# Performance work log

Hardware: AMD Instinct MI355X
Metric: run time of the kernel (lower is better)

The kernel has to match this reference:

```python
import jax, jax.numpy as jnp
import numpy as np

EPS_GN = 1e-5
EPS_ATTN = 1e-6
HEADS = 4
DIM_HEAD = 32
GROUPS = 32  # min(32, channels=128)


def group_norm(x, weight, bias, groups=GROUPS, eps=EPS_GN):
    # x: [b, c, h, w]
    b, c, h, w = x.shape
    xg = x.reshape(b, groups, c // groups, h, w)
    mean = xg.mean(axis=(2, 3, 4), keepdims=True)
    var = xg.var(axis=(2, 3, 4), keepdims=True)
    xg = (xg - mean) * jax.lax.rsqrt(var + eps)
    x = xg.reshape(b, c, h, w)
    return x * weight[None, :, None, None] + bias[None, :, None, None]


def conv1x1(x, w):
    # x: [b, c, h, w], w: [out, in] -> [b, out, h, w]
    return jnp.einsum('bchw,oc->bohw', x, w)


def setup_inputs() -> dict:
    key = jax.random.key(0)
    ks = jax.random.split(key, 6)
    b, c, h, w = 16, 128, 128, 128
    inner = HEADS * DIM_HEAD  # 128
    x = jax.random.normal(ks[0], (b, c, h, w), dtype=jnp.float32)
    gn1_w = jnp.ones((c,), jnp.float32) + 0.02 * jax.random.normal(ks[1], (c,), jnp.float32)
    gn1_b = 0.02 * jax.random.normal(ks[2], (c,), jnp.float32)
    w_qkv = jax.random.normal(ks[3], (inner * 3, c), jnp.float32) / np.sqrt(c)
    w_out = jax.random.normal(ks[4], (c, inner), jnp.float32) / np.sqrt(inner)
    gn2_w = jnp.ones((c,), jnp.float32) + 0.02 * jax.random.normal(ks[5], (c,), jnp.float32)
    gn2_b = jnp.zeros((c,), jnp.float32)
    return {"x": x, "gn1_w": gn1_w, "gn1_b": gn1_b, "w_qkv": w_qkv,
            "w_out": w_out, "gn2_w": gn2_w, "gn2_b": gn2_b}


def reference(x, gn1_w, gn1_b, w_qkv, w_out, gn2_w, gn2_b):
    b, c, h, w = x.shape
    residual = x
    xn = group_norm(x, gn1_w, gn1_b)
    qkv = conv1x1(xn, w_qkv)                      # [b, 3*inner, h, w]
    q, k, v = jnp.split(qkv, 3, axis=1)
    # 'b (heads d) h w -> b heads (h w) d'
    def to_tokens(t):
        return t.reshape(b, HEADS, DIM_HEAD, h * w).transpose(0, 1, 3, 2)
    q, k, v = to_tokens(q), to_tokens(k), to_tokens(v)
    q = jax.nn.elu(q) + 1.0
    k = jax.nn.elu(k) + 1.0
    k_sum = k.sum(axis=2)                          # [b, heads, d]
    kv = jnp.einsum('bhnd,bhne->bhde', k, v)       # [b, heads, d, d]
    qk_sum = jnp.einsum('bhnd,bhd->bhn', q, k_sum) # [b, heads, n]
    qkv_out = jnp.einsum('bhnd,bhde->bhne', q, kv) # [b, heads, n, d]
    out = qkv_out / (qk_sum[..., None] + EPS_ATTN)
    # 'b heads (h w) d -> b (heads d) h w'
    out = out.transpose(0, 1, 3, 2).reshape(b, HEADS * DIM_HEAD, h, w)
    out = conv1x1(out, w_out)
    out = group_norm(out, gn2_w, gn2_b)
    return out + residual
```

## Files before the change

### kernel.cpp

```cpp
#include <hip/hip_runtime.h>

#define B_   16
#define C_   128
#define HW_  16384

typedef __attribute__((ext_vector_type(4))) float  floatx4;
typedef __attribute__((ext_vector_type(8))) short  short8;
typedef __attribute__((ext_vector_type(4))) short  short4v;

static __device__ __forceinline__ unsigned short f2bf(float f){
  unsigned int u = __float_as_uint(f);
  u += 0x7FFFu + ((u >> 16) & 1u);
  return (unsigned short)(u >> 16);
}
static __device__ __forceinline__ float bf2f(unsigned short h){
  return __uint_as_float(((unsigned int)h) << 16);
}
static __device__ __forceinline__ float elu1(float v){
  return v > 0.f ? v + 1.f : __expf(v);
}
static __device__ __forceinline__ int keyx(int n){ return ((n >> 1) & 7) ^ ((n >> 4) & 7); }

__global__ __launch_bounds__(512) void k_xprep(const float* __restrict__ x,
    unsigned short* __restrict__ xT, float* __restrict__ gn1part){
  int blk = blockIdx.x;
  int b = blk >> 6, tile = blk & 63;
  int n0 = tile * 256;
  __shared__ unsigned short XS[32768];
  int t = threadIdx.x, w = t >> 6, l = t & 63;
  float sk[4], sk2[4];
  #pragma unroll
  for (int k = 0; k < 4; ++k){ sk[k] = 0.f; sk2[k] = 0.f; }
  #pragma unroll
  for (int k = 0; k < 4; ++k){
    float4 f4[4];
    #pragma unroll
    for (int j = 0; j < 4; ++j){
      int c = 16*w + 4*k + j;
      f4[j] = *(const float4*)(x + ((size_t)(b*128 + c))*HW_ + n0 + 4*l);
    }
    #pragma unroll
    for (int j = 0; j < 4; ++j){
      sk[k]  += f4[j].x + f4[j].y + f4[j].z + f4[j].w;
      sk2[k] += f4[j].x*f4[j].x + f4[j].y*f4[j].y + f4[j].z*f4[j].z + f4[j].w*f4[j].w;
    }
    int c0 = 16*w + 4*k, cs = c0 >> 3, co = c0 & 7;
    #pragma unroll
    for (int i = 0; i < 4; ++i){
      int n = 4*l + i;
      short4v p;
      #pragma unroll
      for (int j = 0; j < 4; ++j) p[j] = (short)f2bf(((const float*)&f4[j])[i]);
      *(short4v*)(XS + n*128 + (((cs ^ keyx(n)) << 3) + co)) = p;
    }
  }
  #pragma unroll
  for (int k = 0; k < 4; ++k){
    float a = sk[k], q = sk2[k];
    #pragma unroll
    for (int o = 32; o; o >>= 1){ a += __shfl_down(a, o); q += __shfl_down(q, o); }
    if (l == 0){
      gn1part[((size_t)blk)*64 + (4*w + k)*2 + 0] = a;
      gn1part[((size_t)blk)*64 + (4*w + k)*2 + 1] = q;
    }
  }
  __syncthreads();
  unsigned short* dst = xT + ((size_t)blk)*32768;
  for (int it = 0; it < 8; ++it){
    int slot = t + it*512;
    *(short8*)(dst + slot*8) = *(const short8*)(XS + slot*8);
  }
}

__global__ __launch_bounds__(64) void k_gn1fin(const float* __restrict__ gn1part,
    float* __restrict__ mean, float* __restrict__ rstd){
  int bg = blockIdx.x;
  int b = bg >> 5, g = bg & 31, l = threadIdx.x;
  const float* p = gn1part + ((size_t)(b*64 + l))*64 + g*2;
  float s = p[0], s2 = p[1];
  #pragma unroll
  for (int o = 32; o; o >>= 1){ s += __shfl_down(s, o); s2 += __shfl_down(s2, o); }
  if (l == 0){
    float m = s * (1.f/65536.f);
    float var = s2 * (1.f/65536.f) - m*m;
    mean[bg] = m; rstd[bg] = rsqrtf(var + 1e-5f);
  }
}

__global__ __launch_bounds__(64) void k_fold(const float* __restrict__ wqkv, const float* __restrict__ wout,
    const float* __restrict__ g1w, const float* __restrict__ g1b,
    const float* __restrict__ mean, const float* __restrict__ rstd,
    unsigned short* __restrict__ wqp, float* __restrict__ bias, unsigned short* __restrict__ woutb){
  int i = blockIdx.x, l = threadIdx.x;
  if (i < 6144){
    int b = i / 384, o = i % 384;
    float bsum = 0.f;
    #pragma unroll
    for (int j = 0; j < 2; ++j){
      int c = l*2 + j, g = c >> 2;
      float m = mean[b*32 + g], r = rstd[b*32 + g];
      float A  = r * g1w[c];
      float Bc = g1b[c] - m * A;
      float wv = wqkv[o*128 + c];
      wqp[((size_t)(b*384 + o))*128 + c] = f2bf(wv * A);
      bsum += wv * Bc;
    }
    #pragma unroll
    for (int o2 = 32; o2; o2 >>= 1) bsum += __shfl_down(bsum, o2);
    if (l == 0) bias[b*384 + o] = bsum;
  } else {
    int r = i - 6144;
    #pragma unroll
    for (int j = 0; j < 2; ++j){ int c = l*2 + j; woutb[r*128 + c] = f2bf(wout[r*128 + c]); }
  }
}

__global__ __launch_bounds__(512) void k_kv(const unsigned short* __restrict__ xT,
    const unsigned short* __restrict__ wqp, const float* __restrict__ bias,
    float* __restrict__ kvpart, float* __restrict__ ksumpart){
  int blk = blockIdx.x;
  int b = blk >> 7, nt = blk & 127;
  __shared__ unsigned short S[32768];
  int t = threadIdx.x, w = t >> 6, lane = t & 63, lr = lane & 15, lk = lane >> 4;
  const unsigned short* src = xT + ((size_t)(b*64 + (nt >> 1)))*32768 + (nt & 1)*16384;
  for (int it = 0; it < 4; ++it){
    int slot = t + it*512;
    *(short8*)(S + slot*8) = *(const short8*)(src + slot*8);
  }
  __syncthreads();
  short8 afr[2][4]; float biasr[2][4];
  #pragma unroll
  for (int rt = 0; rt < 2; ++rt){
    int o = 128 + rt*128 + w*16;
    #pragma unroll
    for (int ks = 0; ks < 4; ++ks)
      afr[rt][ks] = *(const short8*)(wqp + ((size_t)(b*384 + o + lr))*128 + ks*32 + lk*8);
    #pragma unroll
    for (int r = 0; r < 4; ++r) biasr[rt][r] = bias[b*384 + o + lk*4 + r];
  }
  short4v kpk[8], vpk[8];
  for (int ct = 0; ct < 8; ++ct){
    int nr = ct*16 + lr;
    int kn = keyx(nr);
    short8 bfr[4];
    #pragma unroll
    for (int ks = 0; ks < 4; ++ks)
      bfr[ks] = *(const short8*)(S + nr*128 + (((ks*4 + lk) ^ kn) << 3));
    #pragma unroll
    for (int rt = 0; rt < 2; ++rt){
      floatx4 acc = {0.f,0.f,0.f,0.f};
      #pragma unroll
      for (int ks = 0; ks < 4; ++ks)
        acc = __builtin_amdgcn_mfma_f32_16x16x32_bf16(afr[rt][ks], bfr[ks], acc, 0,0,0);
      short4v pk;
      #pragma unroll
      for (int r = 0; r < 4; ++r){
        float v = acc[r] + biasr[rt][r];
        if (rt == 0) v = elu1(v);
        pk[r] = (short)f2bf(v);
      }
      if (rt == 0) kpk[ct] = pk; else vpk[ct] = pk;
    }
  }
  __syncthreads();
  for (int ct = 0; ct < 8; ++ct){
    int n = ct*16 + lr;
    #pragma unroll
    for (int r = 0; r < 4; ++r){
      int c = w*16 + lk*4 + r;
      int key = (c >> 1) & 7;
      int off = c*128 + ((((n >> 3) ^ key) << 3) + (n & 7));
      S[off]         = (unsigned short)kpk[ct][r];
      S[16384 + off] = (unsigned short)vpk[ct][r];
    }
  }
  __syncthreads();
  short8 ones;
  #pragma unroll
  for (int j = 0; j < 8; ++j) ones[j] = (short)0x3F80;
  #pragma unroll
  for (int j = 0; j < 2; ++j){
    int m = w + 8*j;
    int h = m >> 2, dt = (m >> 1) & 1, et = m & 1;
    int arow = h*32 + dt*16 + lr, brow = h*32 + et*16 + lr;
    int akey = (lr >> 1) & 7;
    floatx4 acc = {0.f,0.f,0.f,0.f}, ks_acc = {0.f,0.f,0.f,0.f};
    #pragma unroll
    for (int ks = 0; ks < 4; ++ks){
      short8 ka = *(const short8*)(S + arow*128 + (((ks*4 + lk) ^ akey) << 3));
      short8 vb = *(const short8*)(S + 16384 + brow*128 + (((ks*4 + lk) ^ akey) << 3));
      acc = __builtin_amdgcn_mfma_f32_16x16x32_bf16(ka, vb, acc, 0,0,0);
      if (et == 0) ks_acc = __builtin_amdgcn_mfma_f32_16x16x32_bf16(ka, ones, ks_acc, 0,0,0);
    }
    float* kvp = kvpart + ((size_t)((b*128 + nt)*4 + h))*1024;
    #pragma unroll
    for (int r = 0; r < 4; ++r)
      kvp[(dt*16 + lk*4 + r)*32 + et*16 + lr] = acc[r];
    if (et == 0 && lr == 0){
      float* ksp = ksumpart + ((size_t)((b*128 + nt)*4 + h))*32;
      #pragma unroll
      for (int r = 0; r < 4; ++r) ksp[dt*16 + lk*4 + r] = ks_acc[r];
    }
  }
}

__global__ __launch_bounds__(256) void k_kvmfold(const float* __restrict__ kvpart, const float* __restrict__ ksumpart,
    const unsigned short* __restrict__ woutb, unsigned short* __restrict__ Mb, float* __restrict__ ksumF){
  int bh = blockIdx.x, t = threadIdx.x;
  int b = bh >> 2, h = bh & 3;
  __shared__ float kvL[1024];
  for (int i = t; i < 1024; i += 256){
    float s = 0.f;
    for (int nt = 0; nt < 128; ++nt) s += kvpart[((size_t)((b*128 + nt)*4 + h))*1024 + i];
    kvL[i] = s;
  }
  if (t < 32){
    float s = 0.f;
    for (int nt = 0; nt < 128; ++nt) s += ksumpart[((size_t)((b*128 + nt)*4 + h))*32 + t];
    ksumF[b*128 + h*32 + t] = s;
  }
  __syncthreads();
  int o = t >> 1, d0 = (t & 1)*16;
  float w2row[32];
  #pragma unroll
  for (int e = 0; e < 32; ++e) w2row[e] = bf2f(woutb[o*128 + h*32 + e]);
  for (int dd = 0; dd < 16; ++dd){
    int d = d0 + dd;
    float s = 0.f;
    #pragma unroll
    for (int e = 0; e < 32; ++e) s += w2row[e] * kvL[d*32 + e];
    Mb[((size_t)b)*16384 + o*128 + h*32 + d] = f2bf(s);
  }
}

__global__ __launch_bounds__(256) void k_attn2(const unsigned short* __restrict__ xT,
    const unsigned short* __restrict__ wqp, const float* __restrict__ bias,
    const float* __restrict__ ksumF, const unsigned short* __restrict__ Mb,
    unsigned short* __restrict__ hbT, float* __restrict__ gn2part){
  int blk = blockIdx.x;
  int b = blk >> 7, t128 = blk & 127;
  __shared__ unsigned short S[16384];
  int t = threadIdx.x, w = t >> 6, lane = t & 63, lr = lane & 15, lk = lane >> 4;
  int rg = w >> 1, cg = w & 1;
  const unsigned short* src = xT + ((size_t)(b*64 + (t128 >> 1)))*32768 + (t128 & 1)*16384;
  for (int it = 0; it < 8; ++it){
    int slot = t + it*256;
    *(short8*)(S + slot*8) = *(const short8*)(src + slot*8);
  }
  short8 afr[4][4]; float biasq[4][4], ksL[4][4];
  #pragma unroll
  for (int rtl = 0; rtl < 4; ++rtl){
    int o = rg*64 + rtl*16;
    #pragma unroll
    for (int ks = 0; ks < 4; ++ks)
      afr[rtl][ks] = *(const short8*)(wqp + ((size_t)(b*384 + o + lr))*128 + ks*32 + lk*8);
    #pragma unroll
    for (int r = 0; r < 4; ++r){
      biasq[rtl][r] = bias[b*384 + o + lk*4 + r];
      ksL[rtl][r]   = ksumF[b*128 + o + lk*4 + r];
    }
  }
  __syncthreads();
  short4v qpk[4][4];
  #pragma unroll
  for (int ctl = 0; ctl < 4; ++ctl){
    int nr = cg*64 + ctl*16 + lr;
    int kn = keyx(nr);
    short8 bfr[4];
    #pragma unroll
    for (int ks = 0; ks < 4; ++ks)
      bfr[ks] = *(const short8*)(S + nr*128 + (((ks*4 + lk) ^ kn) << 3));
    float qv[4][4];
    #pragma unroll
    for (int rtl = 0; rtl < 4; ++rtl){
      floatx4 acc = {0.f,0.f,0.f,0.f};
      #pragma unroll
      for (int ks = 0; ks < 4; ++ks)
        acc = __builtin_amdgcn_mfma_f32_16x16x32_bf16(afr[rtl][ks], bfr[ks], acc, 0,0,0);
      #pragma unroll
      for (int r = 0; r < 4; ++r) qv[rtl][r] = elu1(acc[r] + biasq[rtl][r]);
    }
    #pragma unroll
    for (int hh = 0; hh < 2; ++hh){
      float p = 0.f;
      #pragma unroll
      for (int rr = 0; rr < 2; ++rr)
        #pragma unroll
        for (int r = 0; r < 4; ++r) p += ksL[2*hh + rr][r] * qv[2*hh + rr][r];
      p += __shfl_xor(p, 16);
      p += __shfl_xor(p, 32);
      float inv = 1.f / (p + 1e-6f);
      #pragma unroll
      for (int rr = 0; rr < 2; ++rr)
        #pragma unroll
        for (int r = 0; r < 4; ++r) qpk[2*hh + rr][ctl][r] = (short)f2bf(qv[2*hh + rr][r] * inv);
    }
  }
  __syncthreads();
  #pragma unroll
  for (int rtl = 0; rtl < 4; ++rtl){
    int c0 = rg*64 + rtl*16 + lk*4;
    #pragma unroll
    for (int ctl = 0; ctl < 4; ++ctl){
      int n = cg*64 + ctl*16 + lr;
      *(short4v*)(S + n*128 + ((((c0 >> 3) ^ (n & 7)) << 3) + (c0 & 7))) = qpk[rtl][ctl];
    }
  }
  __syncthreads();
  short8 afr2[4][4];
  #pragma unroll
  for (int rtl = 0; rtl < 4; ++rtl)
    #pragma unroll
    for (int ks = 0; ks < 4; ++ks)
      afr2[rtl][ks] = *(const short8*)(Mb + ((size_t)b)*16384 + (size_t)(rg*64 + rtl*16 + lr)*128 + ks*32 + lk*8);
  float gs[4][4], gq[4][4];
  #pragma unroll
  for (int rtl = 0; rtl < 4; ++rtl)
    #pragma unroll
    for (int r = 0; r < 4; ++r){ gs[rtl][r] = 0.f; gq[rtl][r] = 0.f; }
  #pragma unroll
  for (int ctl = 0; ctl < 4; ++ctl){
    int nr = cg*64 + ctl*16 + lr;
    short8 bfr[4];
    #pragma unroll
    for (int ks = 0; ks < 4; ++ks)
      bfr[ks] = *(const short8*)(S + nr*128 + (((ks*4 + lk) ^ (nr & 7)) << 3));
    #pragma unroll
    for (int rtl = 0; rtl < 4; ++rtl){
      floatx4 acc = {0.f,0.f,0.f,0.f};
      #pragma unroll
      for (int ks = 0; ks < 4; ++ks)
        acc = __builtin_amdgcn_mfma_f32_16x16x32_bf16(afr2[rtl][ks], bfr[ks], acc, 0,0,0);
      #pragma unroll
      for (int r = 0; r < 4; ++r){
        float hv = acc[r];
        int c = rg*64 + rtl*16 + lk*4 + r;
        hbT[(size_t)blk*16384 + c*128 + nr] = f2bf(hv);
        gs[rtl][r] += hv; gq[rtl][r] += hv * hv;
      }
    }
  }
  #pragma unroll
  for (int m = 1; m < 16; m <<= 1)
    #pragma unroll
    for (int rtl = 0; rtl < 4; ++rtl)
      #pragma unroll
      for (int r = 0; r < 4; ++r){ gs[rtl][r] += __shfl_xor(gs[rtl][r], m); gq[rtl][r] += __shfl_xor(gq[rtl][r], m); }
  if (lr == 0){
    #pragma unroll
    for (int rtl = 0; rtl < 4; ++rtl)
      #pragma unroll
      for (int r = 0; r < 4; ++r){
        int c = rg*64 + rtl*16 + lk*4 + r;
        gn2part[((size_t)(blk*2 + cg)*128 + c)*2 + 0] = gs[rtl][r];
        gn2part[((size_t)(blk*2 + cg)*128 + c)*2 + 1] = gq[rtl][r];
      }
  }
}

__global__ __launch_bounds__(64) void k_gn2stats(const float* __restrict__ gn2part,
    float* __restrict__ mean, float* __restrict__ rstd){
  int b = blockIdx.x >> 5, g = blockIdx.x & 31;
  int lane = threadIdx.x;
  float s = 0.f, s2 = 0.f;
  #pragma unroll
  for (int tt = 0; tt < 2; ++tt){
    int t128 = lane + tt*64;
    #pragma unroll
    for (int cgi = 0; cgi < 2; ++cgi)
      #pragma unroll
      for (int j = 0; j < 4; ++j){
        const float* p = gn2part + ((size_t)((b*128 + t128)*2 + cgi)*128 + g*4 + j)*2;
        s += p[0]; s2 += p[1];
      }
  }
  #pragma unroll
  for (int o = 32; o; o >>= 1){ s += __shfl_down(s, o); s2 += __shfl_down(s2, o); }
  if (lane == 0){
    float m = s * (1.f/65536.f);
    float var = s2 * (1.f/65536.f) - m*m;
    mean[blockIdx.x] = m; rstd[blockIdx.x] = rsqrtf(var + 1e-5f);
  }
}

__global__ __launch_bounds__(256) void k_final(const unsigned short* __restrict__ hbT,
    const unsigned short* __restrict__ xT, float* __restrict__ out,
    const float* __restrict__ mean, const float* __restrict__ rstd,
    const float* __restrict__ g2w, const float* __restrict__ g2b){
  int blk = blockIdx.x;
  int b = blk >> 7, t128 = blk & 127;
  __shared__ unsigned short XS[16384];
  int t = threadIdx.x;
  const unsigned short* src = xT + ((size_t)(b*64 + (t128 >> 1)))*32768 + (t128 & 1)*16384;
  for (int it = 0; it < 8; ++it){
    int slot = t + it*256;
    *(short8*)(XS + slot*8) = *(const short8*)(src + slot*8);
  }
  __syncthreads();
  const unsigned short* hsrc = hbT + (size_t)blk*16384;
  for (int it = 0; it < 8; ++it){
    int idx = t + it*256;
    int c = idx >> 4, oct = idx & 15;
    int bg = b*32 + (c >> 2);
    float m = mean[bg], r = rstd[bg];
    float sc = r * g2w[c], sh = g2b[c] - m * sc;
    short8 hv = *(const short8*)(hsrc + c*128 + oct*8);
    float ov[8];
    #pragma unroll
    for (int j = 0; j < 8; ++j){
      int n = oct*8 + j;
      unsigned short xv = XS[n*128 + ((((c >> 3) ^ keyx(n)) << 3) + (c & 7))];
      ov[j] = bf2f((unsigned short)hv[j])*sc + sh + bf2f(xv);
    }
    float* op = out + ((size_t)(b*128 + c))*HW_ + t128*128 + oct*8;
    float4 o0, o1;
    o0.x = ov[0]; o0.y = ov[1]; o0.z = ov[2]; o0.w = ov[3];
    o1.x = ov[4]; o1.y = ov[5]; o1.z = ov[6]; o1.w = ov[7];
    *(float4*)op = o0; *(float4*)(op + 4) = o1;
  }
}

extern "C" void kernel_launch(void* const* d_in, const int* in_sizes, int n_in,
                              void* d_out, int out_size, void* d_ws, size_t ws_size,
                              hipStream_t stream){
  const float* x    = (const float*)d_in[0];
  const float* g1w  = (const float*)d_in[1];
  const float* g1b  = (const float*)d_in[2];
  const float* wqkv = (const float*)d_in[3];
  const float* wout = (const float*)d_in[4];
  const float* g2w  = (const float*)d_in[5];
  const float* g2b  = (const float*)d_in[6];
  char* ws = (char*)d_ws;
  (void)in_sizes; (void)n_in; (void)out_size; (void)ws_size;

  float* gn1part  = (float*)(ws + 0);
  float* gn1_mean = (float*)(ws + 262144);
  float* gn1_rstd = (float*)(ws + 264192);
  float* gn2_mean = (float*)(ws + 266240);
  float* gn2_rstd = (float*)(ws + 268288);
  float* bias     = (float*)(ws + 270336);
  unsigned short* woutb = (unsigned short*)(ws + 294912);
  float* ksumF    = (float*)(ws + 327680);
  unsigned short* Mb = (unsigned short*)(ws + 335872);
  unsigned short* wqp = (unsigned short*)(ws + 860160);
  float* ksumpart = (float*)(ws + 2433024);
  float* kvpart   = (float*)(ws + 4194304);
  float* gn2part  = (float*)(ws + 37748736);
  unsigned short* xT  = (unsigned short*)(ws + 41943040);
  unsigned short* hbT = (unsigned short*)(ws + 109051904);

  k_xprep<<<dim3(1024), dim3(512), 0, stream>>>(x, xT, gn1part);
  k_gn1fin<<<dim3(512), dim3(64), 0, stream>>>(gn1part, gn1_mean, gn1_rstd);
  k_fold<<<dim3(6272), dim3(64), 0, stream>>>(wqkv, wout, g1w, g1b, gn1_mean, gn1_rstd, wqp, bias, woutb);
  k_kv<<<dim3(2048), dim3(512), 0, stream>>>(xT, wqp, bias, kvpart, ksumpart);
  k_kvmfold<<<dim3(64), dim3(256), 0, stream>>>(kvpart, ksumpart, woutb, Mb, ksumF);
  k_attn2<<<dim3(2048), dim3(256), 0, stream>>>(xT, wqp, bias, ksumF, Mb, hbT, gn2part);
  k_gn2stats<<<dim3(512), dim3(64), 0, stream>>>(gn2part, gn2_mean, gn2_rstd);
  k_final<<<dim3(2048), dim3(256), 0, stream>>>(hbT, xT, (float*)d_out, gn2_mean, gn2_rstd, g2w, g2b);
}
```

Before: 241.1 us.

## Restructure attn2 so each wave owns 32 tokens and drops shared-memory staging

k_attn2 now gives each wave its own 32 token columns across all 128 channels. It reads its B fragments straight from global xT and moves the normalized q between MFMA layouts with lane shuffles, so the shared-memory round trip and the block barriers go away. The hbT output is written in an MFMA-fragment layout with vectorized short4 stores instead of scattered 2-byte stores, and k_final stages hbT through shared memory to undo that layout. Per-wave GN2 partials grow to four rows per block, which changes the k_gn2stats indexing and the workspace offsets. In exchange, every wave reloads the full wqp and Mb weight matrices, and k_final uses twice the shared memory.

```diff
diff --git a/kernel.cpp b/kernel.cpp
--- a/kernel.cpp
+++ b/kernel.cpp
@@ -7,6 +7,8 @@
 typedef __attribute__((ext_vector_type(4))) float  floatx4;
 typedef __attribute__((ext_vector_type(8))) short  short8;
 typedef __attribute__((ext_vector_type(4))) short  short4v;
+
+typedef union { unsigned int u[4]; short8 s; } pk8_t;
 
 static __device__ __forceinline__ unsigned short f2bf(float f){
   unsigned int u = __float_as_uint(f);
@@ -15,6 +17,9 @@
 }
 static __device__ __forceinline__ float bf2f(unsigned short h){
   return __uint_as_float(((unsigned int)h) << 16);
+}
+static __device__ __forceinline__ unsigned int pack2bf(float lo, float hi){
+  return (unsigned int)f2bf(lo) | ((unsigned int)f2bf(hi) << 16);
 }
 static __device__ __forceinline__ float elu1(float v){
   return v > 0.f ? v + 1.f : __expf(v);
@@ -239,144 +244,133 @@
     unsigned short* __restrict__ hbT, float* __restrict__ gn2part){
   int blk = blockIdx.x;
   int b = blk >> 7, t128 = blk & 127;
-  __shared__ unsigned short S[16384];
   int t = threadIdx.x, w = t >> 6, lane = t & 63, lr = lane & 15, lk = lane >> 4;
-  int rg = w >> 1, cg = w & 1;
   const unsigned short* src = xT + ((size_t)(b*64 + (t128 >> 1)))*32768 + (t128 & 1)*16384;
-  for (int it = 0; it < 8; ++it){
-    int slot = t + it*256;
-    *(short8*)(S + slot*8) = *(const short8*)(src + slot*8);
-  }
-  short8 afr[4][4]; float biasq[4][4], ksL[4][4];
-  #pragma unroll
-  for (int rtl = 0; rtl < 4; ++rtl){
-    int o = rg*64 + rtl*16;
+
+  short8 xq[2][4];
+  #pragma unroll
+  for (int nt = 0; nt < 2; ++nt){
+    int nr = w*32 + nt*16 + lr;
+    int kn = keyx(nr);
     #pragma unroll
     for (int ks = 0; ks < 4; ++ks)
-      afr[rtl][ks] = *(const short8*)(wqp + ((size_t)(b*384 + o + lr))*128 + ks*32 + lk*8);
-    #pragma unroll
-    for (int r = 0; r < 4; ++r){
-      biasq[rtl][r] = bias[b*384 + o + lk*4 + r];
-      ksL[rtl][r]   = ksumF[b*128 + o + lk*4 + r];
-    }
-  }
-  __syncthreads();
-  short4v qpk[4][4];
-  #pragma unroll
-  for (int ctl = 0; ctl < 4; ++ctl){
-    int nr = cg*64 + ctl*16 + lr;
-    int kn = keyx(nr);
-    short8 bfr[4];
-    #pragma unroll
-    for (int ks = 0; ks < 4; ++ks)
-      bfr[ks] = *(const short8*)(S + nr*128 + (((ks*4 + lk) ^ kn) << 3));
-    float qv[4][4];
-    #pragma unroll
-    for (int rtl = 0; rtl < 4; ++rtl){
-      floatx4 acc = {0.f,0.f,0.f,0.f};
+      xq[nt][ks] = *(const short8*)(src + nr*128 + (((ks*4 + lk) ^ kn) << 3));
+  }
+
+  unsigned int qp[2][8][2];
+  #pragma unroll
+  for (int h = 0; h < 4; ++h){
+    short8 afr[2][4]; float bq_[2][4], ks_[2][4];
+    #pragma unroll
+    for (int rr = 0; rr < 2; ++rr){
+      int rtl = h*2 + rr;
       #pragma unroll
       for (int ks = 0; ks < 4; ++ks)
-        acc = __builtin_amdgcn_mfma_f32_16x16x32_bf16(afr[rtl][ks], bfr[ks], acc, 0,0,0);
-      #pragma unroll
-      for (int r = 0; r < 4; ++r) qv[rtl][r] = elu1(acc[r] + biasq[rtl][r]);
-    }
-    #pragma unroll
-    for (int hh = 0; hh < 2; ++hh){
-      float p = 0.f;
-      #pragma unroll
-      for (int rr = 0; rr < 2; ++rr)
+        afr[rr][ks] = *(const short8*)(wqp + ((size_t)(b*384 + rtl*16 + lr))*128 + ks*32 + lk*8);
+      #pragma unroll
+      for (int r = 0; r < 4; ++r){
+        int c = rtl*16 + lk*4 + r;
+        bq_[rr][r] = bias[b*384 + c];
+        ks_[rr][r] = ksumF[b*128 + c];
+      }
+    }
+    #pragma unroll
+    for (int nt = 0; nt < 2; ++nt){
+      float qv[2][4]; float p = 0.f;
+      #pragma unroll
+      for (int rr = 0; rr < 2; ++rr){
+        floatx4 acc = {0.f,0.f,0.f,0.f};
         #pragma unroll
-        for (int r = 0; r < 4; ++r) p += ksL[2*hh + rr][r] * qv[2*hh + rr][r];
+        for (int ks = 0; ks < 4; ++ks)
+          acc = __builtin_amdgcn_mfma_f32_16x16x32_bf16(afr[rr][ks], xq[nt][ks], acc, 0,0,0);
+        #pragma unroll
+        for (int r = 0; r < 4; ++r){
+          qv[rr][r] = elu1(acc[r] + bq_[rr][r]);
+          p += ks_[rr][r] * qv[rr][r];
+        }
+      }
       p += __shfl_xor(p, 16);
       p += __shfl_xor(p, 32);
       float inv = 1.f / (p + 1e-6f);
       #pragma unroll
-      for (int rr = 0; rr < 2; ++rr)
-        #pragma unroll
-        for (int r = 0; r < 4; ++r) qpk[2*hh + rr][ctl][r] = (short)f2bf(qv[2*hh + rr][r] * inv);
-    }
-  }
-  __syncthreads();
-  #pragma unroll
-  for (int rtl = 0; rtl < 4; ++rtl){
-    int c0 = rg*64 + rtl*16 + lk*4;
-    #pragma unroll
-    for (int ctl = 0; ctl < 4; ++ctl){
-      int n = cg*64 + ctl*16 + lr;
-      *(short4v*)(S + n*128 + ((((c0 >> 3) ^ (n & 7)) << 3) + (c0 & 7))) = qpk[rtl][ctl];
-    }
-  }
-  __syncthreads();
-  short8 afr2[4][4];
-  #pragma unroll
-  for (int rtl = 0; rtl < 4; ++rtl)
+      for (int rr = 0; rr < 2; ++rr){
+        int rtl = h*2 + rr;
+        qp[nt][rtl][0] = pack2bf(qv[rr][0]*inv, qv[rr][1]*inv);
+        qp[nt][rtl][1] = pack2bf(qv[rr][2]*inv, qv[rr][3]*inv);
+      }
+    }
+  }
+
+  short8 bq[2][4];
+  #pragma unroll
+  for (int nt = 0; nt < 2; ++nt)
+    #pragma unroll
+    for (int ks = 0; ks < 4; ++ks){
+      pk8_t pk;
+      #pragma unroll
+      for (int m = 0; m < 4; ++m){
+        int slane = (((lk*2 + (m >> 1)) & 3) << 4) | lr;
+        unsigned int c0 = (unsigned int)__shfl((int)qp[nt][2*ks    ][m & 1], slane);
+        unsigned int c1 = (unsigned int)__shfl((int)qp[nt][2*ks + 1][m & 1], slane);
+        pk.u[m] = (lk & 2) ? c1 : c0;
+      }
+      bq[nt][ks] = pk.s;
+    }
+
+  const unsigned short* mb = Mb + (size_t)b * 16384;
+  float* gpp = gn2part + ((size_t)(blk*4 + w)) * 256;
+  unsigned short* hdst = hbT + (size_t)blk * 16384;
+  #pragma unroll
+  for (int rtl = 0; rtl < 8; ++rtl){
+    short8 afr2[4];
     #pragma unroll
     for (int ks = 0; ks < 4; ++ks)
-      afr2[rtl][ks] = *(const short8*)(Mb + ((size_t)b)*16384 + (size_t)(rg*64 + rtl*16 + lr)*128 + ks*32 + lk*8);
-  float gs[4][4], gq[4][4];
-  #pragma unroll
-  for (int rtl = 0; rtl < 4; ++rtl)
-    #pragma unroll
-    for (int r = 0; r < 4; ++r){ gs[rtl][r] = 0.f; gq[rtl][r] = 0.f; }
-  #pragma unroll
-  for (int ctl = 0; ctl < 4; ++ctl){
-    int nr = cg*64 + ctl*16 + lr;
-    short8 bfr[4];
-    #pragma unroll
-    for (int ks = 0; ks < 4; ++ks)
-      bfr[ks] = *(const short8*)(S + nr*128 + (((ks*4 + lk) ^ (nr & 7)) << 3));
-    #pragma unroll
-    for (int rtl = 0; rtl < 4; ++rtl){
+      afr2[ks] = *(const short8*)(mb + (rtl*16 + lr)*128 + ks*32 + lk*8);
+    float gs[4] = {0,0,0,0}, gq[4] = {0,0,0,0};
+    #pragma unroll
+    for (int nt = 0; nt < 2; ++nt){
       floatx4 acc = {0.f,0.f,0.f,0.f};
       #pragma unroll
       for (int ks = 0; ks < 4; ++ks)
-        acc = __builtin_amdgcn_mfma_f32_16x16x32_bf16(afr2[rtl][ks], bfr[ks], acc, 0,0,0);
+        acc = __builtin_amdgcn_mfma_f32_16x16x32_bf16(afr2[ks], bq[nt][ks], acc, 0,0,0);
+      short4v pk;
       #pragma unroll
       for (int r = 0; r < 4; ++r){
         float hv = acc[r];
-        int c = rg*64 + rtl*16 + lk*4 + r;
-        hbT[(size_t)blk*16384 + c*128 + nr] = f2bf(hv);
-        gs[rtl][r] += hv; gq[rtl][r] += hv * hv;
-      }
-    }
-  }
-  #pragma unroll
-  for (int m = 1; m < 16; m <<= 1)
-    #pragma unroll
-    for (int rtl = 0; rtl < 4; ++rtl)
-      #pragma unroll
-      for (int r = 0; r < 4; ++r){ gs[rtl][r] += __shfl_xor(gs[rtl][r], m); gq[rtl][r] += __shfl_xor(gq[rtl][r], m); }
-  if (lr == 0){
-    #pragma unroll
-    for (int rtl = 0; rtl < 4; ++rtl)
+        pk[r] = (short)f2bf(hv);
+        gs[r] += hv; gq[r] += hv*hv;
+      }
+      *(short4v*)(hdst + (((w*8 + rtl)*2 + nt) << 8) + lane*4) = pk;
+    }
+    #pragma unroll
+    for (int m = 1; m < 16; m <<= 1)
+      #pragma unroll
+      for (int r = 0; r < 4; ++r){ gs[r] += __shfl_xor(gs[r], m); gq[r] += __shfl_xor(gq[r], m); }
+    if (lr == 0){
       #pragma unroll
       for (int r = 0; r < 4; ++r){
-        int c = rg*64 + rtl*16 + lk*4 + r;
-        gn2part[((size_t)(blk*2 + cg)*128 + c)*2 + 0] = gs[rtl][r];
-        gn2part[((size_t)(blk*2 + cg)*128 + c)*2 + 1] = gq[rtl][r];
-      }
+        int c = rtl*16 + lk*4 + r;
+        gpp[c*2 + 0] = gs[r];
+        gpp[c*2 + 1] = gq[r];
+      }
+    }
   }
 }
 
 __global__ __launch_bounds__(64) void k_gn2stats(const float* __restrict__ gn2part,
     float* __restrict__ mean, float* __restrict__ rstd){
   int b = blockIdx.x >> 5, g = blockIdx.x & 31;
-  int lane = threadIdx.x;
+  int l = threadIdx.x;
   float s = 0.f, s2 = 0.f;
-  #pragma unroll
-  for (int tt = 0; tt < 2; ++tt){
-    int t128 = lane + tt*64;
-    #pragma unroll
-    for (int cgi = 0; cgi < 2; ++cgi)
-      #pragma unroll
-      for (int j = 0; j < 4; ++j){
-        const float* p = gn2part + ((size_t)((b*128 + t128)*2 + cgi)*128 + g*4 + j)*2;
-        s += p[0]; s2 += p[1];
-      }
+  for (int rr = 0; rr < 8; ++rr){
+    int row = l + rr*64;
+    const float* p = gn2part + ((size_t)(b*512 + row))*256 + g*8;
+    #pragma unroll
+    for (int j = 0; j < 4; ++j){ s += p[j*2]; s2 += p[j*2 + 1]; }
   }
   #pragma unroll
   for (int o = 32; o; o >>= 1){ s += __shfl_down(s, o); s2 += __shfl_down(s2, o); }
-  if (lane == 0){
+  if (l == 0){
     float m = s * (1.f/65536.f);
     float var = s2 * (1.f/65536.f) - m*m;
     mean[blockIdx.x] = m; rstd[blockIdx.x] = rsqrtf(var + 1e-5f);
@@ -389,28 +383,32 @@
     const float* __restrict__ g2w, const float* __restrict__ g2b){
   int blk = blockIdx.x;
   int b = blk >> 7, t128 = blk & 127;
+  __shared__ unsigned short HS[16384];
   __shared__ unsigned short XS[16384];
   int t = threadIdx.x;
-  const unsigned short* src = xT + ((size_t)(b*64 + (t128 >> 1)))*32768 + (t128 & 1)*16384;
+  const unsigned short* hsrc = hbT + (size_t)blk*16384;
+  const unsigned short* xsrc = xT + ((size_t)(b*64 + (t128 >> 1)))*32768 + (t128 & 1)*16384;
   for (int it = 0; it < 8; ++it){
     int slot = t + it*256;
-    *(short8*)(XS + slot*8) = *(const short8*)(src + slot*8);
-  }
-  __syncthreads();
-  const unsigned short* hsrc = hbT + (size_t)blk*16384;
+    *(short8*)(HS + slot*8) = *(const short8*)(hsrc + slot*8);
+    *(short8*)(XS + slot*8) = *(const short8*)(xsrc + slot*8);
+  }
+  __syncthreads();
   for (int it = 0; it < 8; ++it){
     int idx = t + it*256;
     int c = idx >> 4, oct = idx & 15;
     int bg = b*32 + (c >> 2);
     float m = mean[bg], r = rstd[bg];
     float sc = r * g2w[c], sh = g2b[c] - m * sc;
-    short8 hv = *(const short8*)(hsrc + c*128 + oct*8);
+    int hbase = ((oct >> 2)*8 + (c >> 4))*512 + ((oct >> 1) & 1)*256
+              + ((c >> 2) & 3)*64 + ((oct & 1)*8)*4 + (c & 3);
     float ov[8];
     #pragma unroll
     for (int j = 0; j < 8; ++j){
       int n = oct*8 + j;
+      float hv = bf2f(HS[hbase + j*4]);
       unsigned short xv = XS[n*128 + ((((c >> 3) ^ keyx(n)) << 3) + (c & 7))];
-      ov[j] = bf2f((unsigned short)hv[j])*sc + sh + bf2f(xv);
+      ov[j] = hv*sc + sh + bf2f(xv);
     }
     float* op = out + ((size_t)(b*128 + c))*HW_ + t128*128 + oct*8;
     float4 o0, o1;
@@ -446,8 +444,8 @@
   float* ksumpart = (float*)(ws + 2433024);
   float* kvpart   = (float*)(ws + 4194304);
   float* gn2part  = (float*)(ws + 37748736);
-  unsigned short* xT  = (unsigned short*)(ws + 41943040);
-  unsigned short* hbT = (unsigned short*)(ws + 109051904);
+  unsigned short* xT  = (unsigned short*)(ws + 46137344);
+  unsigned short* hbT = (unsigned short*)(ws + 113246208);
 
   k_xprep<<<dim3(1024), dim3(512), 0, stream>>>(x, xT, gn1part);
   k_gn1fin<<<dim3(512), dim3(64), 0, stream>>>(gn1part, gn1_mean, gn1_rstd);
```

Measured after the change: 256.7 us. 6.5% more time.

## Process two token tiles per attn2 block and write hbT in fragment layout

Applied to the files above, without the earlier changes.

k_attn2 now handles two 128-token tiles per block (1024 blocks), reusing the weight fragments loaded into registers and prefetching the second tile's xT into registers while the first is computed. The hbT output is written as contiguous short4 per-lane fragments instead of scattered 2-byte stores, and k_final stages hbT through LDS and unpacks that layout. The workspace offsets for xT and hbT are shifted. The cost is more LDS per attn2 block (64KB) and more registers, which lowers occupancy, plus an extra LDS buffer in k_final.

```diff
diff --git a/kernel.cpp b/kernel.cpp
--- a/kernel.cpp
+++ b/kernel.cpp
@@ -238,15 +238,21 @@
     const float* __restrict__ ksumF, const unsigned short* __restrict__ Mb,
     unsigned short* __restrict__ hbT, float* __restrict__ gn2part){
   int blk = blockIdx.x;
-  int b = blk >> 7, t128 = blk & 127;
-  __shared__ unsigned short S[16384];
+  int b = blk >> 6, pair = blk & 63;
+  __shared__ unsigned short S[2][16384];
   int t = threadIdx.x, w = t >> 6, lane = t & 63, lr = lane & 15, lk = lane >> 4;
   int rg = w >> 1, cg = w & 1;
-  const unsigned short* src = xT + ((size_t)(b*64 + (t128 >> 1)))*32768 + (t128 & 1)*16384;
-  for (int it = 0; it < 8; ++it){
-    int slot = t + it*256;
-    *(short8*)(S + slot*8) = *(const short8*)(src + slot*8);
-  }
+
+  const unsigned short* src = xT + ((size_t)(b*64 + pair))*32768;
+  #pragma unroll
+  for (int i = 0; i < 8; ++i){
+    short8 v = *(const short8*)(src + (t + i*256)*8);
+    *(short8*)(&S[0][(t + i*256)*8]) = v;
+  }
+  short8 st[8];
+  #pragma unroll
+  for (int i = 0; i < 8; ++i) st[i] = *(const short8*)(src + 16384 + (t + i*256)*8);
+
   short8 afr[4][4]; float biasq[4][4], ksL[4][4];
   #pragma unroll
   for (int rtl = 0; rtl < 4; ++rtl){
@@ -260,101 +266,112 @@
       ksL[rtl][r]   = ksumF[b*128 + o + lk*4 + r];
     }
   }
-  __syncthreads();
-  short4v qpk[4][4];
-  #pragma unroll
-  for (int ctl = 0; ctl < 4; ++ctl){
-    int nr = cg*64 + ctl*16 + lr;
-    int kn = keyx(nr);
-    short8 bfr[4];
-    #pragma unroll
-    for (int ks = 0; ks < 4; ++ks)
-      bfr[ks] = *(const short8*)(S + nr*128 + (((ks*4 + lk) ^ kn) << 3));
-    float qv[4][4];
-    #pragma unroll
-    for (int rtl = 0; rtl < 4; ++rtl){
-      floatx4 acc = {0.f,0.f,0.f,0.f};
-      #pragma unroll
-      for (int ks = 0; ks < 4; ++ks)
-        acc = __builtin_amdgcn_mfma_f32_16x16x32_bf16(afr[rtl][ks], bfr[ks], acc, 0,0,0);
-      #pragma unroll
-      for (int r = 0; r < 4; ++r) qv[rtl][r] = elu1(acc[r] + biasq[rtl][r]);
-    }
-    #pragma unroll
-    for (int hh = 0; hh < 2; ++hh){
-      float p = 0.f;
-      #pragma unroll
-      for (int rr = 0; rr < 2; ++rr)
-        #pragma unroll
-        for (int r = 0; r < 4; ++r) p += ksL[2*hh + rr][r] * qv[2*hh + rr][r];
-      p += __shfl_xor(p, 16);
-      p += __shfl_xor(p, 32);
-      float inv = 1.f / (p + 1e-6f);
-      #pragma unroll
-      for (int rr = 0; rr < 2; ++rr)
-        #pragma unroll
-        for (int r = 0; r < 4; ++r) qpk[2*hh + rr][ctl][r] = (short)f2bf(qv[2*hh + rr][r] * inv);
-    }
-  }
-  __syncthreads();
-  #pragma unroll
-  for (int rtl = 0; rtl < 4; ++rtl){
-    int c0 = rg*64 + rtl*16 + lk*4;
-    #pragma unroll
-    for (int ctl = 0; ctl < 4; ++ctl){
-      int n = cg*64 + ctl*16 + lr;
-      *(short4v*)(S + n*128 + ((((c0 >> 3) ^ (n & 7)) << 3) + (c0 & 7))) = qpk[rtl][ctl];
-    }
-  }
-  __syncthreads();
   short8 afr2[4][4];
   #pragma unroll
   for (int rtl = 0; rtl < 4; ++rtl)
     #pragma unroll
     for (int ks = 0; ks < 4; ++ks)
       afr2[rtl][ks] = *(const short8*)(Mb + ((size_t)b)*16384 + (size_t)(rg*64 + rtl*16 + lr)*128 + ks*32 + lk*8);
-  float gs[4][4], gq[4][4];
-  #pragma unroll
-  for (int rtl = 0; rtl < 4; ++rtl)
-    #pragma unroll
-    for (int r = 0; r < 4; ++r){ gs[rtl][r] = 0.f; gq[rtl][r] = 0.f; }
-  #pragma unroll
-  for (int ctl = 0; ctl < 4; ++ctl){
-    int nr = cg*64 + ctl*16 + lr;
-    short8 bfr[4];
-    #pragma unroll
-    for (int ks = 0; ks < 4; ++ks)
-      bfr[ks] = *(const short8*)(S + nr*128 + (((ks*4 + lk) ^ (nr & 7)) << 3));
+  __syncthreads();
+
+  for (int tt = 0; tt < 2; ++tt){
+    unsigned short* Sc = &S[tt][0];
+    short4v qpk[4][4];
+    #pragma unroll
+    for (int ctl = 0; ctl < 4; ++ctl){
+      int nr = cg*64 + ctl*16 + lr;
+      int kn = keyx(nr);
+      short8 bfr[4];
+      #pragma unroll
+      for (int ks = 0; ks < 4; ++ks)
+        bfr[ks] = *(const short8*)(Sc + nr*128 + (((ks*4 + lk) ^ kn) << 3));
+      float qv[4][4];
+      #pragma unroll
+      for (int rtl = 0; rtl < 4; ++rtl){
+        floatx4 acc = {0.f,0.f,0.f,0.f};
+        #pragma unroll
+        for (int ks = 0; ks < 4; ++ks)
+          acc = __builtin_amdgcn_mfma_f32_16x16x32_bf16(afr[rtl][ks], bfr[ks], acc, 0,0,0);
+        #pragma unroll
+        for (int r = 0; r < 4; ++r) qv[rtl][r] = elu1(acc[r] + biasq[rtl][r]);
+      }
+      #pragma unroll
+      for (int hh = 0; hh < 2; ++hh){
+        float p = 0.f;
+        #pragma unroll
+        for (int rr = 0; rr < 2; ++rr)
+          #pragma unroll
+          for (int r = 0; r < 4; ++r) p += ksL[2*hh + rr][r] * qv[2*hh + rr][r];
+        p += __shfl_xor(p, 16);
+        p += __shfl_xor(p, 32);
+        float inv = 1.f / (p + 1e-6f);
+        #pragma unroll
+        for (int rr = 0; rr < 2; ++rr)
+          #pragma unroll
+          for (int r = 0; r < 4; ++r) qpk[2*hh + rr][ctl][r] = (short)f2bf(qv[2*hh + rr][r] * inv);
+      }
+    }
+    if (tt == 0){
+      #pragma unroll
+      for (int i = 0; i < 8; ++i) *(short8*)(&S[1][(t + i*256)*8]) = st[i];
+    }
+    __syncthreads();
     #pragma unroll
     for (int rtl = 0; rtl < 4; ++rtl){
-      floatx4 acc = {0.f,0.f,0.f,0.f};
+      int c0 = rg*64 + rtl*16 + lk*4;
+      #pragma unroll
+      for (int ctl = 0; ctl < 4; ++ctl){
+        int n = cg*64 + ctl*16 + lr;
+        *(short4v*)(Sc + n*128 + ((((c0 >> 3) ^ (n & 7)) << 3) + (c0 & 7))) = qpk[rtl][ctl];
+      }
+    }
+    __syncthreads();
+    int t128g = pair*2 + tt;
+    unsigned short* hdst = hbT + ((size_t)(b*128 + t128g))*16384;
+    float gs[4][4], gq[4][4];
+    #pragma unroll
+    for (int rtl = 0; rtl < 4; ++rtl)
+      #pragma unroll
+      for (int r = 0; r < 4; ++r){ gs[rtl][r] = 0.f; gq[rtl][r] = 0.f; }
+    #pragma unroll
+    for (int ctl = 0; ctl < 4; ++ctl){
+      int nr = cg*64 + ctl*16 + lr;
+      short8 bfr[4];
       #pragma unroll
       for (int ks = 0; ks < 4; ++ks)
-        acc = __builtin_amdgcn_mfma_f32_16x16x32_bf16(afr2[rtl][ks], bfr[ks], acc, 0,0,0);
-      #pragma unroll
-      for (int r = 0; r < 4; ++r){
-        float hv = acc[r];
-        int c = rg*64 + rtl*16 + lk*4 + r;
-        hbT[(size_t)blk*16384 + c*128 + nr] = f2bf(hv);
-        gs[rtl][r] += hv; gq[rtl][r] += hv * hv;
-      }
-    }
-  }
-  #pragma unroll
-  for (int m = 1; m < 16; m <<= 1)
-    #pragma unroll
-    for (int rtl = 0; rtl < 4; ++rtl)
-      #pragma unroll
-      for (int r = 0; r < 4; ++r){ gs[rtl][r] += __shfl_xor(gs[rtl][r], m); gq[rtl][r] += __shfl_xor(gq[rtl][r], m); }
-  if (lr == 0){
-    #pragma unroll
-    for (int rtl = 0; rtl < 4; ++rtl)
-      #pragma unroll
-      for (int r = 0; r < 4; ++r){
-        int c = rg*64 + rtl*16 + lk*4 + r;
-        gn2part[((size_t)(blk*2 + cg)*128 + c)*2 + 0] = gs[rtl][r];
-        gn2part[((size_t)(blk*2 + cg)*128 + c)*2 + 1] = gq[rtl][r];
-      }
+        bfr[ks] = *(const short8*)(Sc + nr*128 + (((ks*4 + lk) ^ (nr & 7)) << 3));
+      #pragma unroll
+      for (int rtl = 0; rtl < 4; ++rtl){
+        floatx4 acc = {0.f,0.f,0.f,0.f};
+        #pragma unroll
+        for (int ks = 0; ks < 4; ++ks)
+          acc = __builtin_amdgcn_mfma_f32_16x16x32_bf16(afr2[rtl][ks], bfr[ks], acc, 0,0,0);
+        short4v pk;
+        #pragma unroll
+        for (int r = 0; r < 4; ++r){
+          float hv = acc[r];
+          pk[r] = (short)f2bf(hv);
+          gs[rtl][r] += hv; gq[rtl][r] += hv*hv;
+        }
+        *(short4v*)(hdst + ((((rg*4 + rtl)*2 + cg)*4 + ctl)*64 + lane)*4) = pk;
+      }
+    }
+    #pragma unroll
+    for (int m = 1; m < 16; m <<= 1)
+      #pragma unroll
+      for (int rtl = 0; rtl < 4; ++rtl)
+        #pragma unroll
+        for (int r = 0; r < 4; ++r){ gs[rtl][r] += __shfl_xor(gs[rtl][r], m); gq[rtl][r] += __shfl_xor(gq[rtl][r], m); }
+    if (lr == 0){
+      #pragma unroll
+      for (int rtl = 0; rtl < 4; ++rtl)
+        #pragma unroll
+        for (int r = 0; r < 4; ++r){
+          int c = rg*64 + rtl*16 + lk*4 + r;
+          gn2part[((size_t)((b*128 + t128g)*2 + cg)*128 + c)*2 + 0] = gs[rtl][r];
+          gn2part[((size_t)((b*128 + t128g)*2 + cg)*128 + c)*2 + 1] = gq[rtl][r];
+        }
+    }
   }
 }
 
@@ -389,28 +406,32 @@
     const float* __restrict__ g2w, const float* __restrict__ g2b){
   int blk = blockIdx.x;
   int b = blk >> 7, t128 = blk & 127;
+  __shared__ unsigned short HS[16384];
   __shared__ unsigned short XS[16384];
   int t = threadIdx.x;
-  const unsigned short* src = xT + ((size_t)(b*64 + (t128 >> 1)))*32768 + (t128 & 1)*16384;
+  const unsigned short* hsrc = hbT + (size_t)blk*16384;
+  const unsigned short* xsrc = xT + ((size_t)(b*64 + (t128 >> 1)))*32768 + (t128 & 1)*16384;
   for (int it = 0; it < 8; ++it){
     int slot = t + it*256;
-    *(short8*)(XS + slot*8) = *(const short8*)(src + slot*8);
-  }
-  __syncthreads();
-  const unsigned short* hsrc = hbT + (size_t)blk*16384;
+    *(short8*)(HS + slot*8) = *(const short8*)(hsrc + slot*8);
+    *(short8*)(XS + slot*8) = *(const short8*)(xsrc + slot*8);
+  }
+  __syncthreads();
   for (int it = 0; it < 8; ++it){
     int idx = t + it*256;
     int c = idx >> 4, oct = idx & 15;
     int bg = b*32 + (c >> 2);
     float m = mean[bg], r = rstd[bg];
     float sc = r * g2w[c], sh = g2b[c] - m * sc;
-    short8 hv = *(const short8*)(hsrc + c*128 + oct*8);
+    int hbase = ((((c >> 4)*2 + (oct >> 3))*4 + ((oct >> 1) & 3))*64
+              + ((c >> 2) & 3)*16 + (oct & 1)*8)*4 + (c & 3);
     float ov[8];
     #pragma unroll
     for (int j = 0; j < 8; ++j){
       int n = oct*8 + j;
+      float hv = bf2f(HS[hbase + j*4]);
       unsigned short xv = XS[n*128 + ((((c >> 3) ^ keyx(n)) << 3) + (c & 7))];
-      ov[j] = bf2f((unsigned short)hv[j])*sc + sh + bf2f(xv);
+      ov[j] = hv*sc + sh + bf2f(xv);
     }
     float* op = out + ((size_t)(b*128 + c))*HW_ + t128*128 + oct*8;
     float4 o0, o1;
@@ -446,15 +467,15 @@
   float* ksumpart = (float*)(ws + 2433024);
   float* kvpart   = (float*)(ws + 4194304);
   float* gn2part  = (float*)(ws + 37748736);
-  unsigned short* xT  = (unsigned short*)(ws + 41943040);
-  unsigned short* hbT = (unsigned short*)(ws + 109051904);
+  unsigned short* xT  = (unsigned short*)(ws + 46137344);
+  unsigned short* hbT = (unsigned short*)(ws + 113246208);
 
   k_xprep<<<dim3(1024), dim3(512), 0, stream>>>(x, xT, gn1part);
   k_gn1fin<<<dim3(512), dim3(64), 0, stream>>>(gn1part, gn1_mean, gn1_rstd);
   k_fold<<<dim3(6272), dim3(64), 0, stream>>>(wqkv, wout, g1w, g1b, gn1_mean, gn1_rstd, wqp, bias, woutb);
   k_kv<<<dim3(2048), dim3(512), 0, stream>>>(xT, wqp, bias, kvpart, ksumpart);
   k_kvmfold<<<dim3(64), dim3(256), 0, stream>>>(kvpart, ksumpart, woutb, Mb, ksumF);
-  k_attn2<<<dim3(2048), dim3(256), 0, stream>>>(xT, wqp, bias, ksumF, Mb, hbT, gn2part);
+  k_attn2<<<dim3(1024), dim3(256), 0, stream>>>(xT, wqp, bias, ksumF, Mb, hbT, gn2part);
   k_gn2stats<<<dim3(512), dim3(64), 0, stream>>>(gn2part, gn2_mean, gn2_rstd);
   k_final<<<dim3(2048), dim3(256), 0, stream>>>(hbT, xT, (float*)d_out, gn2_mean, gn2_rstd, g2w, g2b);
 }
```

New measurement: 250.9 us. +4.0%, slower.

## Retile attention kernel to 256-token blocks with fragment-layout coalesced output

Applied to the files above, without the earlier changes.

k_attn2 now handles a 256-token tile per 512-thread block, with 64 KB of shared memory. The q computation is split over four row groups and two column groups. In the output stage each wave owns 16 output channels across all 256 tokens, so it loads a single Mb fragment. hbT is written in MFMA fragment order as contiguous short4 stores instead of scattered 2-byte stores. k_final stages that layout through a new shared buffer, and gn2stats reads half as many partials. The change trades lower block count and higher LDS use per block, which may reduce occupancy, for coalesced stores and less fragment reloading.

```diff
diff --git a/kernel.cpp b/kernel.cpp
--- a/kernel.cpp
+++ b/kernel.cpp
@@ -233,24 +233,24 @@
   }
 }
 
-__global__ __launch_bounds__(256) void k_attn2(const unsigned short* __restrict__ xT,
+__global__ __launch_bounds__(512) void k_attn2(const unsigned short* __restrict__ xT,
     const unsigned short* __restrict__ wqp, const float* __restrict__ bias,
     const float* __restrict__ ksumF, const unsigned short* __restrict__ Mb,
     unsigned short* __restrict__ hbT, float* __restrict__ gn2part){
   int blk = blockIdx.x;
-  int b = blk >> 7, t128 = blk & 127;
-  __shared__ unsigned short S[16384];
+  int b = blk >> 6;
+  __shared__ unsigned short S[32768];
   int t = threadIdx.x, w = t >> 6, lane = t & 63, lr = lane & 15, lk = lane >> 4;
-  int rg = w >> 1, cg = w & 1;
-  const unsigned short* src = xT + ((size_t)(b*64 + (t128 >> 1)))*32768 + (t128 & 1)*16384;
+  int rg = w & 3, cg = w >> 2;
+  const unsigned short* src = xT + ((size_t)blk)*32768;
   for (int it = 0; it < 8; ++it){
-    int slot = t + it*256;
+    int slot = t + it*512;
     *(short8*)(S + slot*8) = *(const short8*)(src + slot*8);
   }
-  short8 afr[4][4]; float biasq[4][4], ksL[4][4];
-  #pragma unroll
-  for (int rtl = 0; rtl < 4; ++rtl){
-    int o = rg*64 + rtl*16;
+  short8 afr[2][4]; float biasq[2][4], ksL[2][4];
+  #pragma unroll
+  for (int rtl = 0; rtl < 2; ++rtl){
+    int o = rg*32 + rtl*16;
     #pragma unroll
     for (int ks = 0; ks < 4; ++ks)
       afr[rtl][ks] = *(const short8*)(wqp + ((size_t)(b*384 + o + lr))*128 + ks*32 + lk*8);
@@ -261,18 +261,17 @@
     }
   }
   __syncthreads();
-  short4v qpk[4][4];
-  #pragma unroll
-  for (int ctl = 0; ctl < 4; ++ctl){
-    int nr = cg*64 + ctl*16 + lr;
+  short4v qpk[2][8];
+  for (int ct = 0; ct < 8; ++ct){
+    int nr = cg*128 + ct*16 + lr;
     int kn = keyx(nr);
     short8 bfr[4];
     #pragma unroll
     for (int ks = 0; ks < 4; ++ks)
       bfr[ks] = *(const short8*)(S + nr*128 + (((ks*4 + lk) ^ kn) << 3));
-    float qv[4][4];
-    #pragma unroll
-    for (int rtl = 0; rtl < 4; ++rtl){
+    float qv[2][4];
+    #pragma unroll
+    for (int rtl = 0; rtl < 2; ++rtl){
       floatx4 acc = {0.f,0.f,0.f,0.f};
       #pragma unroll
       for (int ks = 0; ks < 4; ++ks)
@@ -280,81 +279,69 @@
       #pragma unroll
       for (int r = 0; r < 4; ++r) qv[rtl][r] = elu1(acc[r] + biasq[rtl][r]);
     }
-    #pragma unroll
-    for (int hh = 0; hh < 2; ++hh){
-      float p = 0.f;
-      #pragma unroll
-      for (int rr = 0; rr < 2; ++rr)
-        #pragma unroll
-        for (int r = 0; r < 4; ++r) p += ksL[2*hh + rr][r] * qv[2*hh + rr][r];
-      p += __shfl_xor(p, 16);
-      p += __shfl_xor(p, 32);
-      float inv = 1.f / (p + 1e-6f);
-      #pragma unroll
-      for (int rr = 0; rr < 2; ++rr)
-        #pragma unroll
-        for (int r = 0; r < 4; ++r) qpk[2*hh + rr][ctl][r] = (short)f2bf(qv[2*hh + rr][r] * inv);
-    }
-  }
-  __syncthreads();
-  #pragma unroll
-  for (int rtl = 0; rtl < 4; ++rtl){
-    int c0 = rg*64 + rtl*16 + lk*4;
-    #pragma unroll
-    for (int ctl = 0; ctl < 4; ++ctl){
-      int n = cg*64 + ctl*16 + lr;
-      *(short4v*)(S + n*128 + ((((c0 >> 3) ^ (n & 7)) << 3) + (c0 & 7))) = qpk[rtl][ctl];
-    }
-  }
-  __syncthreads();
-  short8 afr2[4][4];
-  #pragma unroll
-  for (int rtl = 0; rtl < 4; ++rtl)
-    #pragma unroll
-    for (int ks = 0; ks < 4; ++ks)
-      afr2[rtl][ks] = *(const short8*)(Mb + ((size_t)b)*16384 + (size_t)(rg*64 + rtl*16 + lr)*128 + ks*32 + lk*8);
-  float gs[4][4], gq[4][4];
-  #pragma unroll
-  for (int rtl = 0; rtl < 4; ++rtl)
-    #pragma unroll
-    for (int r = 0; r < 4; ++r){ gs[rtl][r] = 0.f; gq[rtl][r] = 0.f; }
-  #pragma unroll
-  for (int ctl = 0; ctl < 4; ++ctl){
-    int nr = cg*64 + ctl*16 + lr;
+    float p = 0.f;
+    #pragma unroll
+    for (int rtl = 0; rtl < 2; ++rtl)
+      #pragma unroll
+      for (int r = 0; r < 4; ++r) p += ksL[rtl][r] * qv[rtl][r];
+    p += __shfl_xor(p, 16);
+    p += __shfl_xor(p, 32);
+    float inv = 1.f / (p + 1e-6f);
+    #pragma unroll
+    for (int rtl = 0; rtl < 2; ++rtl){
+      short4v pk;
+      #pragma unroll
+      for (int r = 0; r < 4; ++r) pk[r] = (short)f2bf(qv[rtl][r] * inv);
+      qpk[rtl][ct] = pk;
+    }
+  }
+  short8 afr2[4];
+  #pragma unroll
+  for (int ks = 0; ks < 4; ++ks)
+    afr2[ks] = *(const short8*)(Mb + ((size_t)b)*16384 + (size_t)(w*16 + lr)*128 + ks*32 + lk*8);
+  __syncthreads();
+  #pragma unroll
+  for (int rtl = 0; rtl < 2; ++rtl){
+    int c0 = rg*32 + rtl*16 + lk*4;
+    #pragma unroll
+    for (int ct = 0; ct < 8; ++ct){
+      int n = cg*128 + ct*16 + lr;
+      *(short4v*)(S + n*128 + ((((c0 >> 3) ^ (n & 7)) << 3) + (c0 & 7))) = qpk[rtl][ct];
+    }
+  }
+  __syncthreads();
+  unsigned short* hdst = hbT + ((size_t)blk)*32768;
+  float gs[4] = {0,0,0,0}, gq[4] = {0,0,0,0};
+  for (int ct = 0; ct < 16; ++ct){
+    int nr = ct*16 + lr;
     short8 bfr[4];
     #pragma unroll
     for (int ks = 0; ks < 4; ++ks)
       bfr[ks] = *(const short8*)(S + nr*128 + (((ks*4 + lk) ^ (nr & 7)) << 3));
-    #pragma unroll
-    for (int rtl = 0; rtl < 4; ++rtl){
-      floatx4 acc = {0.f,0.f,0.f,0.f};
-      #pragma unroll
-      for (int ks = 0; ks < 4; ++ks)
-        acc = __builtin_amdgcn_mfma_f32_16x16x32_bf16(afr2[rtl][ks], bfr[ks], acc, 0,0,0);
-      #pragma unroll
-      for (int r = 0; r < 4; ++r){
-        float hv = acc[r];
-        int c = rg*64 + rtl*16 + lk*4 + r;
-        hbT[(size_t)blk*16384 + c*128 + nr] = f2bf(hv);
-        gs[rtl][r] += hv; gq[rtl][r] += hv * hv;
-      }
-    }
+    floatx4 acc = {0.f,0.f,0.f,0.f};
+    #pragma unroll
+    for (int ks = 0; ks < 4; ++ks)
+      acc = __builtin_amdgcn_mfma_f32_16x16x32_bf16(afr2[ks], bfr[ks], acc, 0,0,0);
+    short4v pk;
+    #pragma unroll
+    for (int r = 0; r < 4; ++r){
+      float hv = acc[r];
+      pk[r] = (short)f2bf(hv);
+      gs[r] += hv; gq[r] += hv*hv;
+    }
+    *(short4v*)(hdst + (w*16 + ct)*256 + lane*4) = pk;
   }
   #pragma unroll
   for (int m = 1; m < 16; m <<= 1)
     #pragma unroll
-    for (int rtl = 0; rtl < 4; ++rtl)
-      #pragma unroll
-      for (int r = 0; r < 4; ++r){ gs[rtl][r] += __shfl_xor(gs[rtl][r], m); gq[rtl][r] += __shfl_xor(gq[rtl][r], m); }
+    for (int r = 0; r < 4; ++r){ gs[r] += __shfl_xor(gs[r], m); gq[r] += __shfl_xor(gq[r], m); }
   if (lr == 0){
     #pragma unroll
-    for (int rtl = 0; rtl < 4; ++rtl)
-      #pragma unroll
-      for (int r = 0; r < 4; ++r){
-        int c = rg*64 + rtl*16 + lk*4 + r;
-        gn2part[((size_t)(blk*2 + cg)*128 + c)*2 + 0] = gs[rtl][r];
-        gn2part[((size_t)(blk*2 + cg)*128 + c)*2 + 1] = gq[rtl][r];
-      }
+    for (int r = 0; r < 4; ++r){
+      int c = w*16 + lk*4 + r;
+      gn2part[((size_t)blk*128 + c)*2 + 0] = gs[r];
+      gn2part[((size_t)blk*128 + c)*2 + 1] = gq[r];
+    }
   }
 }
 
@@ -364,15 +351,9 @@
   int lane = threadIdx.x;
   float s = 0.f, s2 = 0.f;
   #pragma unroll
-  for (int tt = 0; tt < 2; ++tt){
-    int t128 = lane + tt*64;
-    #pragma unroll
-    for (int cgi = 0; cgi < 2; ++cgi)
-      #pragma unroll
-      for (int j = 0; j < 4; ++j){
-        const float* p = gn2part + ((size_t)((b*128 + t128)*2 + cgi)*128 + g*4 + j)*2;
-        s += p[0]; s2 += p[1];
-      }
+  for (int j = 0; j < 4; ++j){
+    const float* p = gn2part + (((size_t)(b*64 + lane))*128 + g*4 + j)*2;
+    s += p[0]; s2 += p[1];
   }
   #pragma unroll
   for (int o = 32; o; o >>= 1){ s += __shfl_down(s, o); s2 += __shfl_down(s2, o); }
@@ -389,28 +370,33 @@
     const float* __restrict__ g2w, const float* __restrict__ g2b){
   int blk = blockIdx.x;
   int b = blk >> 7, t128 = blk & 127;
+  int tile = t128 >> 1, half = t128 & 1;
+  __shared__ unsigned short HS[16384];
   __shared__ unsigned short XS[16384];
   int t = threadIdx.x;
-  const unsigned short* src = xT + ((size_t)(b*64 + (t128 >> 1)))*32768 + (t128 & 1)*16384;
+  const unsigned short* hsrc = hbT + ((size_t)(b*64 + tile))*32768;
+  const unsigned short* xsrc = xT + ((size_t)(b*64 + tile))*32768 + half*16384;
   for (int it = 0; it < 8; ++it){
     int slot = t + it*256;
-    *(short8*)(XS + slot*8) = *(const short8*)(src + slot*8);
-  }
-  __syncthreads();
-  const unsigned short* hsrc = hbT + (size_t)blk*16384;
+    int w8 = slot >> 8, rest = slot & 255;
+    *(short8*)(HS + slot*8) = *(const short8*)(hsrc + ((w8*16 + half*8)*256 + rest*8));
+    *(short8*)(XS + slot*8) = *(const short8*)(xsrc + slot*8);
+  }
+  __syncthreads();
   for (int it = 0; it < 8; ++it){
     int idx = t + it*256;
     int c = idx >> 4, oct = idx & 15;
     int bg = b*32 + (c >> 2);
     float m = mean[bg], r = rstd[bg];
     float sc = r * g2w[c], sh = g2b[c] - m * sc;
-    short8 hv = *(const short8*)(hsrc + c*128 + oct*8);
+    int hbase0 = ((c >> 4)*8 + (oct >> 1))*256 + ((c >> 2) & 3)*64 + (oct & 1)*32 + (c & 3);
     float ov[8];
     #pragma unroll
     for (int j = 0; j < 8; ++j){
       int n = oct*8 + j;
+      float hv = bf2f(HS[hbase0 + j*4]);
       unsigned short xv = XS[n*128 + ((((c >> 3) ^ keyx(n)) << 3) + (c & 7))];
-      ov[j] = bf2f((unsigned short)hv[j])*sc + sh + bf2f(xv);
+      ov[j] = hv*sc + sh + bf2f(xv);
     }
     float* op = out + ((size_t)(b*128 + c))*HW_ + t128*128 + oct*8;
     float4 o0, o1;
@@ -446,15 +432,15 @@
   float* ksumpart = (float*)(ws + 2433024);
   float* kvpart   = (float*)(ws + 4194304);
   float* gn2part  = (float*)(ws + 37748736);
-  unsigned short* xT  = (unsigned short*)(ws + 41943040);
-  unsigned short* hbT = (unsigned short*)(ws + 109051904);
+  unsigned short* xT  = (unsigned short*)(ws + 46137344);
+  unsigned short* hbT = (unsigned short*)(ws + 113246208);
 
   k_xprep<<<dim3(1024), dim3(512), 0, stream>>>(x, xT, gn1part);
   k_gn1fin<<<dim3(512), dim3(64), 0, stream>>>(gn1part, gn1_mean, gn1_rstd);
   k_fold<<<dim3(6272), dim3(64), 0, stream>>>(wqkv, wout, g1w, g1b, gn1_mean, gn1_rstd, wqp, bias, woutb);
   k_kv<<<dim3(2048), dim3(512), 0, stream>>>(xT, wqp, bias, kvpart, ksumpart);
   k_kvmfold<<<dim3(64), dim3(256), 0, stream>>>(kvpart, ksumpart, woutb, Mb, ksumF);
-  k_attn2<<<dim3(2048), dim3(256), 0, stream>>>(xT, wqp, bias, ksumF, Mb, hbT, gn2part);
+  k_attn2<<<dim3(1024), dim3(512), 0, stream>>>(xT, wqp, bias, ksumF, Mb, hbT, gn2part);
   k_gn2stats<<<dim3(512), dim3(64), 0, stream>>>(gn2part, gn2_mean, gn2_rstd);
   k_final<<<dim3(2048), dim3(256), 0, stream>>>(hbT, xT, (float*)d_out, gn2_mean, gn2_rstd, g2w, g2b);
 }
```

New measurement: 216.5 us. 1.11x faster.
